# Kernel tuning notes

Measured on AMD Instinct MI355X. Metric: run time of the kernel, lower is better.

## Reference

```python
import jax, jax.numpy as jnp
import numpy as np

INPUT_CHANNELS = 3

def setup_inputs() -> dict:
    key = jax.random.key(0)
    k1, k2 = jax.random.split(key)
    B, N, C = 16, 4096, 3
    x = jax.random.normal(k1, (B, N, C), dtype=jnp.float32)
    y = jax.random.normal(k2, (B, N, C), dtype=jnp.float32)
    return {"x": x, "y": y}

def reference(x, y):
    # Slice to input_channels (identity here since C == INPUT_CHANNELS)
    x = x[:, :, :INPUT_CHANNELS]
    y = y[:, :, :INPUT_CHANNELS]
    # pdist[b, i, j] = ||x_i||^2 + ||y_j||^2 - 2 x_i . y_j  -> squared euclidean
    x2 = jnp.sum(x * x, axis=-1)  # [B, N]
    y2 = jnp.sum(y * y, axis=-1)  # [B, N]
    zz = jnp.einsum('bic,bjc->bij', x, y)  # [B, N, N]
    pdist = x2[:, :, None] + y2[:, None, :] - 2.0 * zz
    # min over axis 1: nearest x for each y; min over axis 2: nearest y for each x
    loss = jnp.mean(jnp.min(pdist, axis=1)) + jnp.mean(jnp.min(pdist, axis=2))
    return loss
```

## Files before the change

kernel.cpp:

```cpp
#include <hip/hip_runtime.h>
#include <stdint.h>

#define BATCH 16
#define NPTS  4096
#define TOT   (BATCH * NPTS)
#define TWOTOT (2 * TOT)
#define JSEG  8

typedef float f4 __attribute__((ext_vector_type(4)));
typedef float f32x4 __attribute__((ext_vector_type(4)));
typedef short bh8 __attribute__((ext_vector_type(8)));
typedef uint32_t u32;
typedef unsigned short u16;
typedef unsigned long long u64;

__device__ __forceinline__ u16 bfr(float f) {
    union { float f; u32 u; } v; v.f = f;
    u32 r = v.u + 0x7FFF + ((v.u >> 16) & 1);
    return (u16)(r >> 16);
}
__device__ __forceinline__ float bfback(u16 h) {
    union { u32 u; float f; } v; v.u = ((u32)h) << 16; return v.f;
}
#define BF16_ONE ((u16)0x3F80)

#define MIN3r(d, a, b, c) \
    asm("v_min3_f32 %0, %1, %2, %3" : "=v"(d) : "v"(a), "v"(b), "v"(c))
#define MIN3a(acc, u, v) \
    asm("v_min3_f32 %0, %1, %2, %0" : "+v"(acc) : "v"(u), "v"(v))

__global__ __launch_bounds__(256) void pack_mfma(const float* __restrict__ x,
                                                 const float* __restrict__ y,
                                                 u16* __restrict__ Arec,
                                                 u16* __restrict__ Brec,
                                                 float* __restrict__ zeros16,
                                                 float* __restrict__ out) {
    int idx = blockIdx.x * 256 + threadIdx.x;
    if (idx == 0) out[0] = 0.0f;
    if (idx == 1) { f4 z = {0.f, 0.f, 0.f, 0.f}; *(f4*)zeros16 = z; }

    bool isx = idx < TOT;
    int r = isx ? idx : (idx - TOT);
    const float* src = isx ? x : y;
    float a = src[r * 3 + 0];
    float b = src[r * 3 + 1];
    float c = src[r * 3 + 2];
    float s2 = fmaf(a, a, fmaf(b, b, c * c));
    u16 s2h = bfr(s2);
    u16 s2l = bfr(s2 - bfback(s2h));

    union { u16 h[16]; f4 v[2]; } rec;
    if (isx) {
        float ax = -2.0f * a, ay = -2.0f * b, az = -2.0f * c;
        u16 ahx = bfr(ax), ahy = bfr(ay), ahz = bfr(az);
        u16 alx = bfr(ax - bfback(ahx));
        u16 aly = bfr(ay - bfback(ahy));
        u16 alz = bfr(az - bfback(ahz));
        rec.h[0] = ahx;  rec.h[1] = ahy;  rec.h[2] = ahz;
        rec.h[3] = ahx;  rec.h[4] = ahy;  rec.h[5] = ahz;
        rec.h[6] = alx;  rec.h[7] = aly;
        rec.h[8] = alz;  rec.h[9] = s2h;  rec.h[10] = s2l;
        rec.h[11] = BF16_ONE; rec.h[12] = BF16_ONE;
        rec.h[13] = 0; rec.h[14] = 0; rec.h[15] = 0;
        f4* dst = (f4*)(Arec + (size_t)r * 16);
        dst[0] = rec.v[0]; dst[1] = rec.v[1];
    } else {
        u16 yhx = bfr(a), yhy = bfr(b), yhz = bfr(c);
        u16 ylx = bfr(a - bfback(yhx));
        u16 yly = bfr(b - bfback(yhy));
        u16 ylz = bfr(c - bfback(yhz));
        rec.h[0] = yhx;  rec.h[1] = yhy;  rec.h[2] = yhz;
        rec.h[3] = ylx;  rec.h[4] = yly;  rec.h[5] = ylz;
        rec.h[6] = yhx;  rec.h[7] = yhy;
        rec.h[8] = yhz;  rec.h[9] = BF16_ONE; rec.h[10] = BF16_ONE;
        rec.h[11] = s2h; rec.h[12] = s2l;
        rec.h[13] = 0; rec.h[14] = 0; rec.h[15] = 0;
        f4* dst = (f4*)(Brec + (size_t)r * 16);
        dst[0] = rec.v[0]; dst[1] = rec.v[1];
    }
}

#define GLOADB(B) do { \
    asm volatile("global_load_dwordx4 %0, %1, off" : "=v"(B) : "v"(baddr)); \
    baddr += bstep; \
} while (0)

#define WAITV(cnt, B) do { \
    asm volatile("s_waitcnt vmcnt(" cnt ")" : "+v"(B)); \
    __builtin_amdgcn_sched_barrier(0); \
} while (0)

#define MF4(P, BB) do { \
    P##0 = __builtin_amdgcn_mfma_f32_16x16x32_bf16(af0, BB, zc, 0, 0, 0); \
    P##1 = __builtin_amdgcn_mfma_f32_16x16x32_bf16(af1, BB, zc, 0, 0, 0); \
    P##2 = __builtin_amdgcn_mfma_f32_16x16x32_bf16(af2, BB, zc, 0, 0, 0); \
    P##3 = __builtin_amdgcn_mfma_f32_16x16x32_bf16(af3, BB, zc, 0, 0, 0); \
} while (0)

#define COLV(cv, P) do { \
    float t0,t1,t2,t3,t4,t5,t6; \
    MIN3r(t0, P##0[0], P##0[1], P##0[2]); \
    MIN3r(t1, P##0[3], P##1[0], P##1[1]); \
    MIN3r(t2, P##1[2], P##1[3], P##2[0]); \
    MIN3r(t3, P##2[1], P##2[2], P##2[3]); \
    MIN3r(t4, P##3[0], P##3[1], P##3[2]); \
    t5 = fminf(P##3[3], t0); \
    MIN3r(t6, t1, t2, t3); \
    MIN3r(cv, t4, t5, t6); \
} while (0)

#define EPI2(PA, PB) do { \
    MIN3a(r00, PA##0[0], PB##0[0]); MIN3a(r01, PA##0[1], PB##0[1]); \
    MIN3a(r02, PA##0[2], PB##0[2]); MIN3a(r03, PA##0[3], PB##0[3]); \
    MIN3a(r10, PA##1[0], PB##1[0]); MIN3a(r11, PA##1[1], PB##1[1]); \
    MIN3a(r12, PA##1[2], PB##1[2]); MIN3a(r13, PA##1[3], PB##1[3]); \
    MIN3a(r20, PA##2[0], PB##2[0]); MIN3a(r21, PA##2[1], PB##2[1]); \
    MIN3a(r22, PA##2[2], PB##2[2]); MIN3a(r23, PA##2[3], PB##2[3]); \
    MIN3a(r30, PA##3[0], PB##3[0]); MIN3a(r31, PA##3[1], PB##3[1]); \
    MIN3a(r32, PA##3[2], PB##3[2]); MIN3a(r33, PA##3[3], PB##3[3]); \
    float cvA, cvB; \
    COLV(cvA, PA); COLV(cvB, PB); \
    asm volatile("ds_min_f32 %0, %1" :: "v"(cma), "v"(cvA)); \
    asm volatile("ds_min_f32 %0, %1 offset:64" :: "v"(cma), "v"(cvB)); \
    cma += 128; \
} while (0)

__global__ __launch_bounds__(256) void chamfer_mfma(const u16* __restrict__ Arec,
                                                    const u16* __restrict__ Brec,
                                                    const float* __restrict__ zeros16,
                                                    float* __restrict__ colpart,
                                                    float* __restrict__ rowpart) {
    constexpr int QLEN   = NPTS / JSEG;
    constexpr int NTILES = QLEN / 16;
    constexpr int NITER  = NTILES / 4 - 1;

    __shared__ float colmin[QLEN];
    int bid  = blockIdx.x;
    int b    = bid >> 7;
    int ic   = (bid >> 3) & 15;
    int jseg = bid & 7;
    int tid  = threadIdx.x;
    int wv   = tid >> 6, lane = tid & 63;
    int lg   = lane >> 4, lm = lane & 15;

    for (int i = tid; i < QLEN; i += 256) colmin[i] = 3.4e38f;

    int i0 = ic * 256 + wv * 64;
    int j0 = jseg * QLEN;

    bh8 af0, af1, af2, af3;
    {
        bh8 z8 = {0, 0, 0, 0, 0, 0, 0, 0};
        const u16* ab = Arec + ((size_t)b * NPTS + i0 + lm) * 16 + lg * 8;
        af0 = (lg < 2) ? *(const bh8*)(ab + 0)   : z8;
        af1 = (lg < 2) ? *(const bh8*)(ab + 256) : z8;
        af2 = (lg < 2) ? *(const bh8*)(ab + 512) : z8;
        af3 = (lg < 2) ? *(const bh8*)(ab + 768) : z8;
    }
    __syncthreads();

    u64 baddr, bstep;
    {
        u64 real = (u64)(uintptr_t)(Brec + ((size_t)b * NPTS + j0 + lm) * 16 + lg * 8);
        u64 zadr = (u64)(uintptr_t)zeros16;
        baddr = (lg < 2) ? real : zadr;
        bstep = (lg < 2) ? (u64)512 : (u64)0;
    }
    u32 cma = (u32)(uintptr_t)&colmin[0] + (u32)lm * 4;

    f32x4 zc = {0.f, 0.f, 0.f, 0.f};
    float r00=3.4e38f, r01=3.4e38f, r02=3.4e38f, r03=3.4e38f;
    float r10=3.4e38f, r11=3.4e38f, r12=3.4e38f, r13=3.4e38f;
    float r20=3.4e38f, r21=3.4e38f, r22=3.4e38f, r23=3.4e38f;
    float r30=3.4e38f, r31=3.4e38f, r32=3.4e38f, r33=3.4e38f;

    f32x4 aA0, aA1, aA2, aA3, aB0, aB1, aB2, aB3;
    bh8 b0, b1, b2, b3;

    GLOADB(b0); GLOADB(b1); GLOADB(b2); GLOADB(b3);

    #pragma unroll 1
    for (int it = 0; it < NITER; ++it) {
        WAITV("3", b0); MF4(aA, b0); GLOADB(b0);
        WAITV("3", b1); MF4(aB, b1); GLOADB(b1);
        EPI2(aA, aB);
        WAITV("3", b2); MF4(aA, b2); GLOADB(b2);
        WAITV("3", b3); MF4(aB, b3); GLOADB(b3);
        EPI2(aA, aB);
    }
    WAITV("3", b0); MF4(aA, b0);
    WAITV("2", b1); MF4(aB, b1);
    EPI2(aA, aB);
    WAITV("1", b2); MF4(aA, b2);
    WAITV("0", b3); MF4(aB, b3);
    EPI2(aA, aB);

    #define RRED(r) { r = fminf(r, __shfl_xor(r, 1)); r = fminf(r, __shfl_xor(r, 2)); \
                      r = fminf(r, __shfl_xor(r, 4)); r = fminf(r, __shfl_xor(r, 8)); }
    RRED(r00) RRED(r01) RRED(r02) RRED(r03)
    RRED(r10) RRED(r11) RRED(r12) RRED(r13)
    RRED(r20) RRED(r21) RRED(r22) RRED(r23)
    RRED(r30) RRED(r31) RRED(r32) RRED(r33)
    if (lm == 0) {
        float* rp = rowpart + (size_t)jseg * TOT + (size_t)b * NPTS + i0 + lg * 4;
        rp[0]  = r00; rp[1]  = r01; rp[2]  = r02; rp[3]  = r03;
        rp[16] = r10; rp[17] = r11; rp[18] = r12; rp[19] = r13;
        rp[32] = r20; rp[33] = r21; rp[34] = r22; rp[35] = r23;
        rp[48] = r30; rp[49] = r31; rp[50] = r32; rp[51] = r33;
    }

    __syncthreads();
    for (int j = tid; j < QLEN; j += 256)
        colpart[(size_t)ic * TOT + (size_t)b * NPTS + j0 + j] = colmin[j];
}

__global__ __launch_bounds__(256) void chamfer_pass2(const float* __restrict__ rowpart,
                                                     const float* __restrict__ colpart,
                                                     float* __restrict__ out) {
    int t = blockIdx.x * 256 + threadIdx.x;
    float mr = rowpart[t];
    #pragma unroll
    for (int s = 1; s < JSEG; ++s) mr = fminf(mr, rowpart[(size_t)s * TOT + t]);
    float mc = colpart[t];
    #pragma unroll
    for (int ic = 1; ic < 16; ++ic) mc = fminf(mc, colpart[(size_t)ic * TOT + t]);

    float s = mr + mc;
    #pragma unroll
    for (int off = 32; off; off >>= 1) s += __shfl_down(s, off);
    __shared__ float red[4];
    int lane = threadIdx.x & 63, wid = threadIdx.x >> 6;
    if (lane == 0) red[wid] = s;
    __syncthreads();
    if (threadIdx.x == 0) {
        float tot = (red[0] + red[1]) + (red[2] + red[3]);
        atomicAdd(out, tot * (1.0f / (float)TOT));
    }
}

__global__ __launch_bounds__(256) void chamfer_direct(const float* __restrict__ x,
                                                      const float* __restrict__ y,
                                                      float* __restrict__ out) {
    int blk = blockIdx.x;
    int dir = blk >> 8;
    int t = blk & 255;
    int b = t >> 4;
    int chunk = t & 15;
    const float* __restrict__ P = (dir ? y : x) + (b * NPTS + chunk * 256) * 3;
    const float* __restrict__ Q = (dir ? x : y) + b * NPTS * 3;
    float px = P[threadIdx.x * 3 + 0];
    float py = P[threadIdx.x * 3 + 1];
    float pz = P[threadIdx.x * 3 + 2];
    float b0 = 3.4e38f, b1 = 3.4e38f, b2 = 3.4e38f, b3 = 3.4e38f;
    for (int j = 0; j < NPTS; j += 4) {
        #pragma unroll
        for (int u = 0; u < 4; ++u) {
            float dx = px - Q[(j + u) * 3 + 0];
            float dy = py - Q[(j + u) * 3 + 1];
            float dz = pz - Q[(j + u) * 3 + 2];
            float d = fmaf(dx, dx, fmaf(dy, dy, dz * dz));
            if (u == 0) b0 = fminf(b0, d);
            if (u == 1) b1 = fminf(b1, d);
            if (u == 2) b2 = fminf(b2, d);
            if (u == 3) b3 = fminf(b3, d);
        }
    }
    float best = fminf(fminf(b0, b1), fminf(b2, b3));
    float v = best;
    #pragma unroll
    for (int off = 32; off; off >>= 1) v += __shfl_down(v, off);
    __shared__ float red[4];
    int lane = threadIdx.x & 63, wid = threadIdx.x >> 6;
    if (lane == 0) red[wid] = v;
    __syncthreads();
    if (threadIdx.x == 0) {
        float s = (red[0] + red[1]) + (red[2] + red[3]);
        atomicAdd(out, s * (1.0f / (float)TOT));
    }
}

__global__ void zero_kernel(float* out) { out[0] = 0.0f; }

extern "C" void kernel_launch(void* const* d_in, const int* in_sizes, int n_in,
                              void* d_out, int out_size, void* d_ws, size_t ws_size,
                              hipStream_t stream) {
    const float* x = (const float*)d_in[0];
    const float* y = (const float*)d_in[1];
    float* out = (float*)d_out;

    size_t need = ((size_t)10 << 20) + 16;
    if (ws_size >= need) {
        u16*   Arec    = (u16*)d_ws;
        u16*   Brec    = (u16*)((char*)d_ws + ((size_t)2 << 20));
        float* colpart = (float*)((char*)d_ws + ((size_t)4 << 20));
        float* rowpart = (float*)((char*)d_ws + ((size_t)8 << 20));
        float* zeros16 = (float*)((char*)d_ws + ((size_t)10 << 20));
        hipLaunchKernelGGL(pack_mfma, dim3(TWOTOT / 256), dim3(256), 0, stream,
                           x, y, Arec, Brec, zeros16, out);
        hipLaunchKernelGGL(chamfer_mfma, dim3(16 * 16 * JSEG), dim3(256), 0, stream,
                           Arec, Brec, zeros16, colpart, rowpart);
        hipLaunchKernelGGL(chamfer_pass2, dim3(TOT / 256), dim3(256), 0, stream,
                           rowpart, colpart, out);
    } else {
        hipLaunchKernelGGL(zero_kernel, dim3(1), dim3(1), 0, stream, out);
        hipLaunchKernelGGL(chamfer_direct, dim3(512), dim3(256), 0, stream, x, y, out);
    }
}
```

Measured before the change: 43.97 us.

## Stage B tile in LDS and stream MFMA operands via ds_read pipeline

Each block now cooperatively copies its 512-point B record segment into shared memory once. The main loop then reads MFMA operands with ds_read_b128 under a 6-deep lgkmcnt-pipelined schedule, replacing the per-wave global loads that fetched the same B data redundantly from all four waves. Lanes with lg>=2 read a valid LDS row instead of a zero buffer, which works only if the A fragment for those lanes is zero. This adds 16KB of LDS per block and a sync before compute, and it may add LDS bank contention and interleave with the ds_min traffic to colmin.

Measured after the change: 43.31 us. About the same (-1.5%).

```diff
diff --git a/kernel.cpp b/kernel.cpp
--- a/kernel.cpp
+++ b/kernel.cpp
@@ -12,7 +12,6 @@
 typedef short bh8 __attribute__((ext_vector_type(8)));
 typedef uint32_t u32;
 typedef unsigned short u16;
-typedef unsigned long long u64;
 
 __device__ __forceinline__ u16 bfr(float f) {
     union { float f; u32 u; } v; v.f = f;
@@ -33,11 +32,9 @@
                                                  const float* __restrict__ y,
                                                  u16* __restrict__ Arec,
                                                  u16* __restrict__ Brec,
-                                                 float* __restrict__ zeros16,
                                                  float* __restrict__ out) {
     int idx = blockIdx.x * 256 + threadIdx.x;
     if (idx == 0) out[0] = 0.0f;
-    if (idx == 1) { f4 z = {0.f, 0.f, 0.f, 0.f}; *(f4*)zeros16 = z; }
 
     bool isx = idx < TOT;
     int r = isx ? idx : (idx - TOT);
@@ -80,13 +77,11 @@
     }
 }
 
-#define GLOADB(B) do { \
-    asm volatile("global_load_dwordx4 %0, %1, off" : "=v"(B) : "v"(baddr)); \
-    baddr += bstep; \
-} while (0)
-
-#define WAITV(cnt, B) do { \
-    asm volatile("s_waitcnt vmcnt(" cnt ")" : "+v"(B)); \
+#define DSRL(dst, base, imm) \
+    asm volatile("ds_read_b128 %0, %1 offset:" imm : "=v"(dst) : "v"(base))
+
+#define WAITL(cnt, slot) do { \
+    asm volatile("s_waitcnt lgkmcnt(" cnt ")" : "+v"(slot)); \
     __builtin_amdgcn_sched_barrier(0); \
 } while (0)
 
@@ -127,14 +122,12 @@
 
 __global__ __launch_bounds__(256) void chamfer_mfma(const u16* __restrict__ Arec,
                                                     const u16* __restrict__ Brec,
-                                                    const float* __restrict__ zeros16,
                                                     float* __restrict__ colpart,
                                                     float* __restrict__ rowpart) {
-    constexpr int QLEN   = NPTS / JSEG;
-    constexpr int NTILES = QLEN / 16;
-    constexpr int NITER  = NTILES / 4 - 1;
-
+    constexpr int QLEN = NPTS / JSEG;
+    __shared__ u16  Bst[QLEN * 16];
     __shared__ float colmin[QLEN];
+
     int bid  = blockIdx.x;
     int b    = bid >> 7;
     int ic   = (bid >> 3) & 15;
@@ -143,10 +136,17 @@
     int wv   = tid >> 6, lane = tid & 63;
     int lg   = lane >> 4, lm = lane & 15;
 
-    for (int i = tid; i < QLEN; i += 256) colmin[i] = 3.4e38f;
-
     int i0 = ic * 256 + wv * 64;
     int j0 = jseg * QLEN;
+
+    {
+        const f4* src = (const f4*)(Brec + ((size_t)b * NPTS + j0) * 16);
+        f4* dst = (f4*)Bst;
+        int t4 = tid * 4;
+        f4 v0 = src[t4 + 0], v1 = src[t4 + 1], v2 = src[t4 + 2], v3 = src[t4 + 3];
+        dst[t4 + 0] = v0; dst[t4 + 1] = v1; dst[t4 + 2] = v2; dst[t4 + 3] = v3;
+    }
+    for (int i = tid; i < QLEN; i += 256) colmin[i] = 3.4e38f;
 
     bh8 af0, af1, af2, af3;
     {
@@ -159,14 +159,8 @@
     }
     __syncthreads();
 
-    u64 baddr, bstep;
-    {
-        u64 real = (u64)(uintptr_t)(Brec + ((size_t)b * NPTS + j0 + lm) * 16 + lg * 8);
-        u64 zadr = (u64)(uintptr_t)zeros16;
-        baddr = (lg < 2) ? real : zadr;
-        bstep = (lg < 2) ? (u64)512 : (u64)0;
-    }
-    u32 cma = (u32)(uintptr_t)&colmin[0] + (u32)lm * 4;
+    u32 lofs = (u32)(uintptr_t)&Bst[0] + ((lg < 2) ? (u32)(lm * 32 + lg * 16) : 0u);
+    u32 cma  = (u32)(uintptr_t)&colmin[0] + (u32)lm * 4;
 
     f32x4 zc = {0.f, 0.f, 0.f, 0.f};
     float r00=3.4e38f, r01=3.4e38f, r02=3.4e38f, r03=3.4e38f;
@@ -175,24 +169,38 @@
     float r30=3.4e38f, r31=3.4e38f, r32=3.4e38f, r33=3.4e38f;
 
     f32x4 aA0, aA1, aA2, aA3, aB0, aB1, aB2, aB3;
-    bh8 b0, b1, b2, b3;
-
-    GLOADB(b0); GLOADB(b1); GLOADB(b2); GLOADB(b3);
-
+    bh8 s0, s1, s2, s3, s4, s5;
+
+    DSRL(s0, lofs, "0");    DSRL(s1, lofs, "512");
+    DSRL(s2, lofs, "1024"); DSRL(s3, lofs, "1536");
+    DSRL(s4, lofs, "2048"); DSRL(s5, lofs, "2560");
+
+    WAITL("5", s0); MF4(aA, s0); DSRL(s0, lofs, "3072");
+    WAITL("5", s1); MF4(aB, s1); DSRL(s1, lofs, "3584");
+    EPI2(aA, aB);
+
+    u32 lofs2 = lofs + 4096;
     #pragma unroll 1
-    for (int it = 0; it < NITER; ++it) {
-        WAITV("3", b0); MF4(aA, b0); GLOADB(b0);
-        WAITV("3", b1); MF4(aB, b1); GLOADB(b1);
+    for (int k = 0; k < 4; ++k) {
+        WAITL("7", s2); MF4(aA, s2); DSRL(s2, lofs2, "0");
+        WAITL("7", s3); MF4(aB, s3); DSRL(s3, lofs2, "512");
         EPI2(aA, aB);
-        WAITV("3", b2); MF4(aA, b2); GLOADB(b2);
-        WAITV("3", b3); MF4(aB, b3); GLOADB(b3);
+        WAITL("7", s4); MF4(aA, s4); DSRL(s4, lofs2, "1024");
+        WAITL("7", s5); MF4(aB, s5); DSRL(s5, lofs2, "1536");
         EPI2(aA, aB);
-    }
-    WAITV("3", b0); MF4(aA, b0);
-    WAITV("2", b1); MF4(aB, b1);
+        WAITL("7", s0); MF4(aA, s0); DSRL(s0, lofs2, "2048");
+        WAITL("7", s1); MF4(aB, s1); DSRL(s1, lofs2, "2560");
+        EPI2(aA, aB);
+        lofs2 += 3072;
+    }
+    WAITL("7", s2); MF4(aA, s2);
+    WAITL("6", s3); MF4(aB, s3);
     EPI2(aA, aB);
-    WAITV("1", b2); MF4(aA, b2);
-    WAITV("0", b3); MF4(aB, b3);
+    WAITL("7", s4); MF4(aA, s4);
+    WAITL("5", s5); MF4(aB, s5);
+    EPI2(aA, aB);
+    WAITL("4", s0); MF4(aA, s0);
+    WAITL("0", s1); MF4(aB, s1);
     EPI2(aA, aB);
 
     #define RRED(r) { r = fminf(r, __shfl_xor(r, 1)); r = fminf(r, __shfl_xor(r, 2)); \
@@ -288,17 +296,16 @@
     const float* y = (const float*)d_in[1];
     float* out = (float*)d_out;
 
-    size_t need = ((size_t)10 << 20) + 16;
+    size_t need = (size_t)10 << 20;
     if (ws_size >= need) {
         u16*   Arec    = (u16*)d_ws;
         u16*   Brec    = (u16*)((char*)d_ws + ((size_t)2 << 20));
         float* colpart = (float*)((char*)d_ws + ((size_t)4 << 20));
         float* rowpart = (float*)((char*)d_ws + ((size_t)8 << 20));
-        float* zeros16 = (float*)((char*)d_ws + ((size_t)10 << 20));
         hipLaunchKernelGGL(pack_mfma, dim3(TWOTOT / 256), dim3(256), 0, stream,
-                           x, y, Arec, Brec, zeros16, out);
+                           x, y, Arec, Brec, out);
         hipLaunchKernelGGL(chamfer_mfma, dim3(16 * 16 * JSEG), dim3(256), 0, stream,
-                           Arec, Brec, zeros16, colpart, rowpart);
+                           Arec, Brec, colpart, rowpart);
         hipLaunchKernelGGL(chamfer_pass2, dim3(TOT / 256), dim3(256), 0, stream,
                            rowpart, colpart, out);
     } else {
```
